# Performance work log

Measured on AMD Instinct MI355X. Metric: run time of the kernel, lower is better.

The kernel has to match this reference:

```python
import jax, jax.numpy as jnp
import numpy as np


def setup_inputs() -> dict:
    key = jax.random.key(0)
    k1, k2, k3, k4 = jax.random.split(key, 4)
    B, Cin, H, W = 16, 64, 96, 96
    D, O, KH, KW, S = 100, 256, 3, 3, 3
    x = jax.random.normal(k1, (B, Cin, H, W), dtype=jnp.float32)
    dictionary = jax.random.normal(k2, (D, Cin, KH, KW), dtype=jnp.float32) * 0.05
    lookup_coefficients = jax.random.normal(k3, (O, KH, KW, S), dtype=jnp.float32) * 0.1
    lookup_indices = jax.random.randint(k4, (O, KH, KW, S), 0, D, dtype=jnp.int64)
    return {
        "x": x,
        "dictionary": dictionary,
        "lookup_coefficients": lookup_coefficients,
        "lookup_indices": lookup_indices,
    }


def reference(x, dictionary, lookup_coefficients, lookup_indices):
    # Dense conv with the small dictionary: [B, Cin, H, W] x [D, Cin, kh, kw] -> [B, D, Oh, Ow]
    conv_out = jax.lax.conv_general_dilated(
        x, dictionary,
        window_strides=(1, 1),
        padding=((1, 1), (1, 1)),
        dimension_numbers=("NCHW", "OIHW", "NCHW"),
    )
    O = lookup_coefficients.shape[0]
    D = dictionary.shape[0]
    # Flatten kernel-position and sparsity axes: each (position, slot) contributes
    # coeff * conv_out[:, idx] to output channel o; COO duplicates sum.
    idx = lookup_indices.reshape(O, -1)      # [O, P*S]
    coeff = lookup_coefficients.reshape(O, -1)  # [O, P*S]
    # Scatter-add into a per-output-channel weight over dictionary entries: W[o, d]
    Wmat = jnp.zeros((O, D), dtype=conv_out.dtype).at[jnp.arange(O)[:, None], idx].add(coeff)
    # Gather-weighted-sum == sparse (O x D) matmul against conv_out channels
    out = jnp.einsum("od,bdhw->bohw", Wmat, conv_out)
    return out
```

## Files before the change

### kernel.cpp

```cpp
#include <hip/hip_runtime.h>

#define NB   16
#define CIN  64
#define HH   96
#define WW   96
#define DD   100
#define OO   256
#define NWG  (NB * HH)
#define NCV  (NB * HH * 2)
#define WPAD 50

typedef __attribute__((ext_vector_type(8))) short  bf16x8;
typedef __attribute__((ext_vector_type(4))) float  f32x4;

#define FSWZ(wp) ((((wp) ^ ((wp) >> 3)) & 7) << 4)

static __device__ __forceinline__ unsigned short f32_to_bf16(float f) {
    unsigned int u = __float_as_uint(f);
    u += 0x7FFFu + ((u >> 16) & 1u);
    return (unsigned short)(u >> 16);
}

__global__ __launch_bounds__(256) void prep_kernel(
    const float* __restrict__ x, const float* __restrict__ dict,
    const float* __restrict__ coeff, const int* __restrict__ idx,
    unsigned short* __restrict__ x2, unsigned short* __restrict__ weff2,
    unsigned short* __restrict__ zbuf)
{
    __shared__ unsigned short lds[CIN * 100];
    __shared__ float wrow[DD];
    const int blk = blockIdx.x, tid = threadIdx.x;

    if (blk < NWG) {
        const int b = blk / HH, h = blk % HH;
        for (int it = 0; it < 6; ++it) {
            int i = tid + it * 256;
            int c = i / 24, w4 = i % 24;
            float4 v = *reinterpret_cast<const float4*>(
                x + (((size_t)(b * CIN + c) * HH + h) * WW + w4 * 4));
            ushort4 u;
            u.x = f32_to_bf16(v.x); u.y = f32_to_bf16(v.y);
            u.z = f32_to_bf16(v.z); u.w = f32_to_bf16(v.w);
            *reinterpret_cast<ushort4*>(&lds[c * 100 + w4 * 4]) = u;
        }
        __syncthreads();
        for (int it = 0; it < 6; ++it) {
            int i = tid + it * 256;
            int w = i / 16, c = (i % 16) * 4;
            ushort4 u;
            u.x = lds[(c + 0) * 100 + w];
            u.y = lds[(c + 1) * 100 + w];
            u.z = lds[(c + 2) * 100 + w];
            u.w = lds[(c + 3) * 100 + w];
            *reinterpret_cast<ushort4*>(x2 + (((size_t)(b * HH + h) * WW + w) * CIN + c)) = u;
        }
    } else {
        const int o = blk - NWG;
        if (o == 0 && tid < 8) zbuf[tid] = 0;
        if (tid < DD) wrow[tid] = 0.f;
        __syncthreads();
        if (tid == 0) {
            for (int s = 0; s < 27; ++s) wrow[idx[o * 27 + s]] += coeff[o * 27 + s];
        }
        __syncthreads();
        for (int j = tid; j < 576; j += 256) {
            int kpos = j >> 6, c = j & 63;
            float s = 0.f;
            for (int d = 0; d < DD; ++d)
                s += wrow[d] * dict[d * 576 + c * 9 + kpos];
            int otile = o >> 4, ks = c >> 5;
            int lane8 = (o & 15) | (((c >> 3) & 3) << 4);
            weff2[((size_t)(kpos * 32 + otile * 2 + ks)) * 512 + lane8 * 8 + (c & 7)]
                = f32_to_bf16(s);
        }
    }
}

__global__ __launch_bounds__(512, 4) void conv_kernel(
    const unsigned short* __restrict__ x2,
    const unsigned short* __restrict__ weff2,
    const unsigned short* __restrict__ zbuf,
    float* __restrict__ out)
{
    __shared__ unsigned short xs[3 * WPAD * 64];

    const int wg  = blockIdx.x;
    const int swz = (wg & 7) * (NCV / 8) + (wg >> 3);
    const int b = swz / 192, rem = swz % 192;
    const int h = rem >> 1, ws = (rem & 1) * 48;
    const int tid = threadIdx.x;
    const int lane = tid & 63, wid = tid >> 6;

    char* xsb = reinterpret_cast<char*>(xs);
    const char* x2b = reinterpret_cast<const char*>(x2) + (size_t)b * HH * WW * 128;
    const char* zbp = reinterpret_cast<const char*>(zbuf);

    const unsigned short* wbase = weff2 + (size_t)(wid * 4) * 512 + lane * 8;
    bf16x8 bA[2], bB[2];
#pragma unroll
    for (int n = 0; n < 2; ++n)
        bA[n] = *reinterpret_cast<const bf16x8*>(wbase + (n * 2 + 0) * 512);
#pragma unroll
    for (int n = 0; n < 2; ++n)
        bB[n] = *reinterpret_cast<const bf16x8*>(wbase + (n * 2 + 1) * 512);

#pragma unroll
    for (int it = 0; it < 3; ++it) {
        int chunk = tid + it * 512;
        if (chunk < 1200) {
            int r = chunk / 400, rem2 = chunk % 400;
            int wp = rem2 >> 3, gb = (rem2 & 7) << 4;
            int hp = h - 1 + r, w = ws - 1 + wp;
            const char* src = (w >= 0 && w < WW && hp >= 0 && hp < HH)
                ? x2b + ((size_t)(hp * WW + w) * 128 + (gb ^ FSWZ(wp)))
                : zbp;
            __builtin_amdgcn_global_load_lds(
                (const __attribute__((address_space(1))) void*)src,
                (__attribute__((address_space(3))) void*)(xsb + chunk * 16),
                16, 0, 0);
        }
    }

    f32x4 acc[3][2];
#pragma unroll
    for (int m = 0; m < 3; ++m)
#pragma unroll
        for (int n = 0; n < 2; ++n)
            acc[m][n] = (f32x4){0.f, 0.f, 0.f, 0.f};

    __syncthreads();

    const int l15 = lane & 15;

#pragma unroll
    for (int s = 0; s < 18; ++s) {
        const int kpos = s >> 1, ks = s & 1;
        const int kh = kpos / 3, dw = kpos % 3;
        const int cb = (ks * 32 + (lane >> 4) * 8) * 2;
        bf16x8 a[3];
#pragma unroll
        for (int m = 0; m < 3; ++m) {
            int wpos = m * 16 + l15 + dw;
            a[m] = *reinterpret_cast<const bf16x8*>(
                xsb + kh * 6400 + wpos * 128 + (cb ^ FSWZ(wpos)));
        }
#pragma unroll
        for (int m = 0; m < 3; ++m)
#pragma unroll
            for (int n = 0; n < 2; ++n)
                acc[m][n] = __builtin_amdgcn_mfma_f32_16x16x32_bf16(
                    a[m], (s & 1) ? bB[n] : bA[n], acc[m][n], 0, 0, 0);
        if (s < 16) {
            const int s2 = s + 2;
            const int off = (s2 >> 1) * 32 + (s2 & 1);
#pragma unroll
            for (int n = 0; n < 2; ++n) {
                bf16x8 v = *reinterpret_cast<const bf16x8*>(wbase + (off + n * 2) * 512);
                if ((s & 1) == 0) bA[n] = v; else bB[n] = v;
            }
        }
    }

#pragma unroll
    for (int m = 0; m < 3; ++m)
#pragma unroll
        for (int n = 0; n < 2; ++n) {
            int o = wid * 32 + n * 16 + l15;
            int w = ws + m * 16 + (lane >> 4) * 4;
            *reinterpret_cast<f32x4*>(
                out + (((size_t)(b * OO + o) * HH + h) * WW + w)) = acc[m][n];
        }
}

extern "C" void kernel_launch(void* const* d_in, const int* in_sizes, int n_in,
                              void* d_out, int out_size, void* d_ws, size_t ws_size,
                              hipStream_t stream) {
    const float* x     = (const float*)d_in[0];
    const float* dict  = (const float*)d_in[1];
    const float* coeff = (const float*)d_in[2];
    const int*   idx   = (const int*)d_in[3];
    float* out = (float*)d_out;

    char* ws = (char*)d_ws;
    unsigned short* weff2 = (unsigned short*)ws;
    unsigned short* zbuf  = (unsigned short*)(ws + 294912);
    unsigned short* x2    = (unsigned short*)(ws + 1048576);

    prep_kernel<<<NWG + OO, 256, 0, stream>>>(x, dict, coeff, idx, x2, weff2, zbuf);
    conv_kernel<<<NCV, 512, 0, stream>>>(x2, weff2, zbuf, out);
}
```

Baseline: 80.74 us.

## Retile conv kernel to two output rows by half of output channels per block

Each workgroup now computes two output rows across the full width for 128 output channels, instead of one row by half the width for all 256 channels. Eight waves split as 2 width by 4 channel groups, and each wave accumulates two rows so every B-fragment load feeds twice as many MFMAs. The LDS tile grows to a 4-row by 98-column halo. This lowers redundant halo staging and weight-fragment loads per output, but doubles accumulator registers and LDS use, which may cut occupancy.

```diff
diff --git a/kernel.cpp b/kernel.cpp
--- a/kernel.cpp
+++ b/kernel.cpp
@@ -7,8 +7,7 @@
 #define DD   100
 #define OO   256
 #define NWG  (NB * HH)
-#define NCV  (NB * HH * 2)
-#define WPAD 50
+#define NCV  1536
 
 typedef __attribute__((ext_vector_type(8))) short  bf16x8;
 typedef __attribute__((ext_vector_type(4))) float  f32x4;
@@ -82,20 +81,23 @@
     const unsigned short* __restrict__ zbuf,
     float* __restrict__ out)
 {
-    __shared__ unsigned short xs[3 * WPAD * 64];
+    __shared__ unsigned short xs[4 * 98 * 64];
 
     const int wg  = blockIdx.x;
     const int swz = (wg & 7) * (NCV / 8) + (wg >> 3);
-    const int b = swz / 192, rem = swz % 192;
-    const int h = rem >> 1, ws = (rem & 1) * 48;
+    const int oh = swz & 1;
+    const int rb = swz >> 1;
+    const int b = rb / 48, h0 = (rb % 48) * 2;
     const int tid = threadIdx.x;
     const int lane = tid & 63, wid = tid >> 6;
+    const int wm = wid >> 2, wn = wid & 3;
+    const int l15 = lane & 15;
 
     char* xsb = reinterpret_cast<char*>(xs);
     const char* x2b = reinterpret_cast<const char*>(x2) + (size_t)b * HH * WW * 128;
     const char* zbp = reinterpret_cast<const char*>(zbuf);
 
-    const unsigned short* wbase = weff2 + (size_t)(wid * 4) * 512 + lane * 8;
+    const unsigned short* wbase = weff2 + (size_t)((oh * 8 + wn * 2) * 2) * 512 + lane * 8;
     bf16x8 bA[2], bB[2];
 #pragma unroll
     for (int n = 0; n < 2; ++n)
@@ -105,14 +107,14 @@
         bB[n] = *reinterpret_cast<const bf16x8*>(wbase + (n * 2 + 1) * 512);
 
 #pragma unroll
-    for (int it = 0; it < 3; ++it) {
+    for (int it = 0; it < 7; ++it) {
         int chunk = tid + it * 512;
-        if (chunk < 1200) {
-            int r = chunk / 400, rem2 = chunk % 400;
-            int wp = rem2 >> 3, gb = (rem2 & 7) << 4;
-            int hp = h - 1 + r, w = ws - 1 + wp;
-            const char* src = (w >= 0 && w < WW && hp >= 0 && hp < HH)
-                ? x2b + ((size_t)(hp * WW + w) * 128 + (gb ^ FSWZ(wp)))
+        if (chunk < 3136) {
+            int r = chunk / 784, rem = chunk % 784;
+            int wp = rem >> 3, gb = (rem & 7) << 4;
+            int hp = h0 - 1 + r;
+            const char* src = (wp >= 1 && wp <= 96 && hp >= 0 && hp < HH)
+                ? x2b + ((size_t)(hp * WW + wp - 1) * 128 + (gb ^ FSWZ(wp)))
                 : zbp;
             __builtin_amdgcn_global_load_lds(
                 (const __attribute__((address_space(1))) void*)src,
@@ -121,35 +123,42 @@
         }
     }
 
-    f32x4 acc[3][2];
-#pragma unroll
-    for (int m = 0; m < 3; ++m)
-#pragma unroll
-        for (int n = 0; n < 2; ++n)
-            acc[m][n] = (f32x4){0.f, 0.f, 0.f, 0.f};
+    f32x4 acc[2][3][2];
+#pragma unroll
+    for (int q = 0; q < 2; ++q)
+#pragma unroll
+        for (int m = 0; m < 3; ++m)
+#pragma unroll
+            for (int n = 0; n < 2; ++n)
+                acc[q][m][n] = (f32x4){0.f, 0.f, 0.f, 0.f};
 
     __syncthreads();
 
-    const int l15 = lane & 15;
+    const int wb16 = wm * 48 + l15;
 
 #pragma unroll
     for (int s = 0; s < 18; ++s) {
         const int kpos = s >> 1, ks = s & 1;
         const int kh = kpos / 3, dw = kpos % 3;
         const int cb = (ks * 32 + (lane >> 4) * 8) * 2;
-        bf16x8 a[3];
+        bf16x8 a[2][3];
 #pragma unroll
         for (int m = 0; m < 3; ++m) {
-            int wpos = m * 16 + l15 + dw;
-            a[m] = *reinterpret_cast<const bf16x8*>(
-                xsb + kh * 6400 + wpos * 128 + (cb ^ FSWZ(wpos)));
-        }
-#pragma unroll
-        for (int m = 0; m < 3; ++m)
-#pragma unroll
-            for (int n = 0; n < 2; ++n)
-                acc[m][n] = __builtin_amdgcn_mfma_f32_16x16x32_bf16(
-                    a[m], (s & 1) ? bB[n] : bA[n], acc[m][n], 0, 0, 0);
+            int wpos = wb16 + m * 16 + dw;
+            int rowoff = wpos * 128 + (cb ^ FSWZ(wpos));
+#pragma unroll
+            for (int q = 0; q < 2; ++q)
+                a[q][m] = *reinterpret_cast<const bf16x8*>(
+                    xsb + (kh + q) * 12544 + rowoff);
+        }
+#pragma unroll
+        for (int q = 0; q < 2; ++q)
+#pragma unroll
+            for (int m = 0; m < 3; ++m)
+#pragma unroll
+                for (int n = 0; n < 2; ++n)
+                    acc[q][m][n] = __builtin_amdgcn_mfma_f32_16x16x32_bf16(
+                        a[q][m], (s & 1) ? bB[n] : bA[n], acc[q][m][n], 0, 0, 0);
         if (s < 16) {
             const int s2 = s + 2;
             const int off = (s2 >> 1) * 32 + (s2 & 1);
@@ -162,14 +171,17 @@
     }
 
 #pragma unroll
-    for (int m = 0; m < 3; ++m)
-#pragma unroll
-        for (int n = 0; n < 2; ++n) {
-            int o = wid * 32 + n * 16 + l15;
-            int w = ws + m * 16 + (lane >> 4) * 4;
-            *reinterpret_cast<f32x4*>(
-                out + (((size_t)(b * OO + o) * HH + h) * WW + w)) = acc[m][n];
-        }
+    for (int q = 0; q < 2; ++q)
+#pragma unroll
+        for (int m = 0; m < 3; ++m)
+#pragma unroll
+            for (int n = 0; n < 2; ++n) {
+                int o = oh * 128 + wn * 32 + n * 16 + l15;
+                int w = wm * 48 + m * 16 + (lane >> 4) * 4;
+                *reinterpret_cast<f32x4*>(
+                    out + (((size_t)(b * OO + o) * HH + h0 + q) * WW + w))
+                    = acc[q][m][n];
+            }
 }
 
 extern "C" void kernel_launch(void* const* d_in, const int* in_sizes, int n_in,
```

New measurement: 140.0 us. 73.4% more time.
